# Performance work log

Hardware: AMD Instinct MI355X
Metric: run time of the kernel (lower is better)

The kernel has to match this reference:

```python
import jax, jax.numpy as jnp
import numpy as np

DEPTH, E, F, H, U, I, B = 12, 256, 128, 8, 1000, 1000, 64
HD = E // H  # head dim = 32
N = 2 * F + 1  # seq len = 257


def _ln(x, g, b, eps=1e-5):
    m = jnp.mean(x, axis=-1, keepdims=True)
    v = jnp.var(x, axis=-1, keepdims=True)
    return (x - m) / jnp.sqrt(v + eps) * g + b


def setup_inputs() -> dict:
    key = jax.random.key(0)
    ks = jax.random.split(key, 16)
    s = 0.02  # weight scale for numeric sanity
    inp = {
        "user": jax.random.randint(ks[0], (B, 1), 0, U, dtype=jnp.int64) if jax.config.jax_enable_x64 else jax.random.randint(ks[0], (B, 1), 0, U).astype(jnp.int32),
        "item": jax.random.randint(ks[1], (B, 1), 0, I).astype(jnp.int32),
        "user_table": jax.random.normal(ks[2], (E, U, F), jnp.float32) * s,
        "item_table": jax.random.normal(ks[3], (E, I, F), jnp.float32) * s,
        "cls_token": jax.random.normal(ks[4], (1, 1, E), jnp.float32),
        "positions": jax.random.normal(ks[5], (N, E), jnp.float32) * s,
        "ln1_g": jnp.ones((DEPTH, E), jnp.float32),
        "ln1_b": jnp.zeros((DEPTH, E), jnp.float32),
        "Wq": jax.random.normal(ks[6], (DEPTH, E, E), jnp.float32) * s,
        "bq": jnp.zeros((DEPTH, E), jnp.float32),
        "Wk": jax.random.normal(ks[7], (DEPTH, E, E), jnp.float32) * s,
        "bk": jnp.zeros((DEPTH, E), jnp.float32),
        "Wv": jax.random.normal(ks[8], (DEPTH, E, E), jnp.float32) * s,
        "bv": jnp.zeros((DEPTH, E), jnp.float32),
        "Wo": jax.random.normal(ks[9], (DEPTH, E, E), jnp.float32) * s,
        "bo": jnp.zeros((DEPTH, E), jnp.float32),
        "ln2_g": jnp.ones((DEPTH, E), jnp.float32),
        "ln2_b": jnp.zeros((DEPTH, E), jnp.float32),
        "W1": jax.random.normal(ks[10], (DEPTH, E, 4 * E), jnp.float32) * s,
        "b1": jnp.zeros((DEPTH, 4 * E), jnp.float32),
        "W2": jax.random.normal(ks[11], (DEPTH, 4 * E, E), jnp.float32) * s,
        "b2": jnp.zeros((DEPTH, E), jnp.float32),
        "head_g": jnp.ones((E,), jnp.float32),
        "head_b": jnp.zeros((E,), jnp.float32),
        "head_W": jax.random.normal(ks[12], (E, 1), jnp.float32) * s,
        "head_bias": jnp.zeros((1,), jnp.float32),
    }
    return inp


def _forward(user, item, user_table, item_table, cls_token, positions,
             ln1_g, ln1_b, Wq, bq, Wk, bk, Wv, bv, Wo, bo,
             ln2_g, ln2_b, W1, b1, W2, b2, head_g, head_b, head_W, head_bias):
    uid = user[:, 0]
    iid = item[:, 0]
    b = uid.shape[0]
    # emb_size parallel embedding lookups, cat over table axis, then transpose:
    # x_user[b, f, e] = user_table[e, uid[b], f]  -> (b, F, E)
    xu = jnp.transpose(user_table[:, uid, :], (1, 2, 0))
    xi = jnp.transpose(item_table[:, iid, :], (1, 2, 0))
    cls = jnp.broadcast_to(cls_token, (b, 1, E))
    x = jnp.concatenate([cls, xu, xi], axis=1) + positions  # (b, N, E)

    def block(x, p):
        g1, be1, wq, bq_, wk, bk_, wv, bv_, wo, bo_, g2, be2, w1, bb1, w2, bb2 = p
        h = _ln(x, g1, be1)

        def heads(w, bias):
            y = h @ w + bias  # (b, N, E)
            return y.reshape(b, N, H, HD).transpose(0, 2, 1, 3)  # (b, H, N, HD)

        q, k, v = heads(wq, bq_), heads(wk, bk_), heads(wv, bv_)
        energy = jnp.einsum('bhqd,bhkd->bhqk', q, k)  # NOTE: unscaled pre-softmax
        att = jax.nn.softmax(energy, axis=-1) / jnp.sqrt(jnp.float32(E))  # post-softmax scaling quirk
        o = jnp.einsum('bhqk,bhkd->bhqd', att, v)
        o = o.transpose(0, 2, 1, 3).reshape(b, N, E)
        x = x + (o @ wo + bo_)
        h2 = _ln(x, g2, be2)
        ff = jax.nn.gelu(h2 @ w1 + bb1, approximate=False) @ w2 + bb2
        return x + ff, None

    x, _ = jax.lax.scan(block, x, (ln1_g, ln1_b, Wq, bq, Wk, bk, Wv, bv, Wo, bo,
                                   ln2_g, ln2_b, W1, b1, W2, b2))
    pooled = jnp.mean(x, axis=1)  # (b, E)
    return _ln(pooled, head_g, head_b) @ head_W + head_bias  # (b, 1)


def reference(user, item, user_table, item_table, cls_token, positions,
              ln1_g, ln1_b, Wq, bq, Wk, bk, Wv, bv, Wo, bo,
              ln2_g, ln2_b, W1, b1, W2, b2, head_g, head_b, head_W, head_bias):
    return _forward(user, item, user_table, item_table, cls_token, positions,
                    ln1_g, ln1_b, Wq, bq, Wk, bk, Wv, bv, Wo, bo,
                    ln2_g, ln2_b, W1, b1, W2, b2, head_g, head_b, head_W, head_bias)
```

## Files before the change

kernel.cpp:

```cpp
#include <hip/hip_runtime.h>
#include <hip/hip_fp16.h>
#include <math.h>

constexpr int DEPTH = 12;
constexpr int E     = 256;
constexpr int H     = 8;
constexpr int HD    = 32;
constexpr int N     = 257;
constexpr int B     = 64;
constexpr int BN    = B * N;
constexpr int BNP   = 16512;
constexpr int FFD   = 1024;
constexpr int UCNT  = 1000;
constexpr int Fdim  = 128;

enum { EPI_RESID = 1, EPI_GELU = 2, EPI_QKV = 3 };

typedef _Float16 f16x8 __attribute__((ext_vector_type(8)));
typedef _Float16 f16x4 __attribute__((ext_vector_type(4)));
typedef float    f32x4 __attribute__((ext_vector_type(4)));

__device__ __forceinline__ float gelu_exact(float z) {
  return 0.5f * z * (1.0f + erff(z * 0.70710678118654752440f));
}

#define GLOAD_LDS16(g, l) __builtin_amdgcn_global_load_lds( \
    (const __attribute__((address_space(1))) void*)(g),     \
    (__attribute__((address_space(3))) void*)(l), 16, 0, 0)

__global__ __launch_bounds__(256) void embed_kernel(
    const int* __restrict__ user, const int* __restrict__ item,
    const float* __restrict__ utab, const float* __restrict__ itab,
    const float* __restrict__ pos, float* __restrict__ x)
{
  __shared__ float tile[32][33];
  const int tx = threadIdx.x, ty = threadIdx.y;
  const int b  = blockIdx.z;
  const int e0 = blockIdx.x * 32;
  const int ft = blockIdx.y;
  const bool isU = (ft < 4);
  const int f0 = (ft & 3) * 32;
  const int id = isU ? user[b] : item[b];
  const float* tab = isU ? utab : itab;
  const int nbase = isU ? 1 : 1 + Fdim;
#pragma unroll
  for (int r = 0; r < 4; ++r) {
    const int e = ty + r * 8;
    tile[e][tx] = tab[((size_t)(e0 + e) * UCNT + id) * Fdim + f0 + tx];
  }
  __syncthreads();
#pragma unroll
  for (int r = 0; r < 4; ++r) {
    const int f = ty + r * 8;
    const int n = nbase + f0 + f;
    x[((size_t)b * N + n) * E + e0 + tx] = tile[tx][f] + pos[(size_t)n * E + e0 + tx];
  }
}

__global__ __launch_bounds__(256) void cls_pad_kernel(
    const float* __restrict__ cls, const float* __restrict__ pos,
    float* __restrict__ x, __half* __restrict__ h)
{
  const int t = blockIdx.x * 256 + threadIdx.x;
  if (blockIdx.y == 0) {
    const int b = t >> 8, e = t & 255;
    x[((size_t)b * N) * E + e] = cls[e] + pos[e];
  } else {
    h[(size_t)BN * E + t] = __float2half(0.0f);
  }
}

__global__ __launch_bounds__(256) void convT_kernel(
    const float* __restrict__ in, __half* __restrict__ out,
    int K, int NC, int NCtot, int ncoff)
{
  __shared__ float tile[32][33];
  const int tx = threadIdx.x, ty = threadIdx.y;
  const int n0 = blockIdx.x * 32, k0 = blockIdx.y * 32;
  const float* ip = in + (size_t)blockIdx.z * K * NC;
  __half* op = out + (size_t)blockIdx.z * NCtot * K;
#pragma unroll
  for (int r = 0; r < 4; ++r) {
    const int kk = ty + r * 8;
    tile[kk][tx] = ip[(size_t)(k0 + kk) * NC + n0 + tx];
  }
  __syncthreads();
#pragma unroll
  for (int r = 0; r < 4; ++r) {
    const int nn = ty + r * 8;
    op[(size_t)(ncoff + n0 + nn) * K + k0 + tx] = __float2half(tile[tx][nn]);
  }
}

__global__ __launch_bounds__(256) void ln_kernel(
    const float* __restrict__ x, __half* __restrict__ y,
    const float* __restrict__ g, const float* __restrict__ b)
{
  const int wave = threadIdx.x >> 6, lane = threadIdx.x & 63;
  const int row  = blockIdx.x * 4 + wave;
  const float4 v = *(const float4*)(x + (size_t)row * E + lane * 4);
  float s = v.x + v.y + v.z + v.w;
  float q = v.x * v.x + v.y * v.y + v.z * v.z + v.w * v.w;
#pragma unroll
  for (int o = 32; o > 0; o >>= 1) { s += __shfl_xor(s, o); q += __shfl_xor(q, o); }
  const float mean = s * (1.0f / 256.0f);
  const float var  = q * (1.0f / 256.0f) - mean * mean;
  const float rstd = rsqrtf(var + 1e-5f);
  const float4 gg = *(const float4*)(g + lane * 4);
  const float4 bb = *(const float4*)(b + lane * 4);
  __half2 h0 = __floats2half2_rn((v.x - mean) * rstd * gg.x + bb.x,
                                 (v.y - mean) * rstd * gg.y + bb.y);
  __half2 h1 = __floats2half2_rn((v.z - mean) * rstd * gg.z + bb.z,
                                 (v.w - mean) * rstd * gg.w + bb.w);
  __half2* yp = (__half2*)(y + (size_t)row * E + lane * 4);
  yp[0] = h0; yp[1] = h1;
}

template<int BMC, int BNT, int K, int NCOUT, int EPI>
__global__ __launch_bounds__(256) void gemm_f16(
    const __half* __restrict__ Act, const __half* __restrict__ Wt,
    const float* __restrict__ b0, const float* __restrict__ b1,
    const float* __restrict__ b2, void* __restrict__ outp)
{
  static_assert(BMC == 128, "col tile fixed at 128");
  constexpr int NT  = BNT / 32;
  constexpr int BSEG = BNT / 16;
  constexpr int BPW  = BSEG / 4;

  __shared__ __half Ws[128 * 32];
  __shared__ __half Bs[BNT * 32];

  const int t = threadIdx.x;
  const int wave = t >> 6, lane = t & 63;
  const int lm = lane & 15, lq = lane >> 4;
  const int col0 = blockIdx.x * BMC;
  const int tok0 = blockIdx.y * BNT;

  const int srow = lane >> 2, sp = lane & 3;
  const __half* wg[2]; __half* wl[2];
#pragma unroll
  for (int i = 0; i < 2; ++i) {
    const int seg = wave * 2 + i;
    const int row = seg * 16 + srow;
    const int slot = sp ^ ((row >> 1) & 3);
    wg[i] = Wt + (size_t)(col0 + row) * K + slot * 8;
    wl[i] = &Ws[seg * 512];
  }
  const __half* ag[BPW]; __half* al[BPW];
#pragma unroll
  for (int i = 0; i < BPW; ++i) {
    const int seg = wave * BPW + i;
    const int row = seg * 16 + srow;
    const int slot = sp ^ ((row >> 1) & 3);
    ag[i] = Act + (size_t)(tok0 + row) * K + slot * 8;
    al[i] = &Bs[seg * 512];
  }

  const int wm = (wave >> 1) * 64;
  const int wn = (wave & 1) * (BNT / 2);

  f32x4 acc[4][NT];
#pragma unroll
  for (int i = 0; i < 4; ++i)
#pragma unroll
    for (int j = 0; j < NT; ++j) acc[i][j] = (f32x4){0.f, 0.f, 0.f, 0.f};

  for (int k0 = 0; k0 < K; k0 += 32) {
#pragma unroll
    for (int i = 0; i < 2; ++i)   GLOAD_LDS16(wg[i] + k0, wl[i]);
#pragma unroll
    for (int i = 0; i < BPW; ++i) GLOAD_LDS16(ag[i] + k0, al[i]);
    __syncthreads();

    f16x8 af[4], bf[NT];
#pragma unroll
    for (int mt = 0; mt < 4; ++mt) {
      const int row = wm + mt * 16 + lm;
      af[mt] = *(const f16x8*)&Ws[row * 32 + (lq ^ ((row >> 1) & 3)) * 8];
    }
#pragma unroll
    for (int nt = 0; nt < NT; ++nt) {
      const int row = wn + nt * 16 + lm;
      bf[nt] = *(const f16x8*)&Bs[row * 32 + (lq ^ ((row >> 1) & 3)) * 8];
    }
#pragma unroll
    for (int mt = 0; mt < 4; ++mt)
#pragma unroll
      for (int nt = 0; nt < NT; ++nt)
        acc[mt][nt] = __builtin_amdgcn_mfma_f32_16x16x32_f16(af[mt], bf[nt], acc[mt][nt], 0, 0, 0);
    __syncthreads();
  }

  float br[4][4];
#pragma unroll
  for (int mt = 0; mt < 4; ++mt) {
    const int cg = col0 + wm + mt * 16 + lq * 4;
    const float* bp;
    if constexpr (EPI == EPI_QKV) {
      const int tsel = cg >> 8;
      bp = (tsel == 0) ? b0 : (tsel == 1 ? b1 : b2);
      bp += (cg & 255);
    } else {
      bp = b0 + cg;
    }
    const float4 bv = *(const float4*)bp;
    br[mt][0] = bv.x; br[mt][1] = bv.y; br[mt][2] = bv.z; br[mt][3] = bv.w;
  }

#pragma unroll
  for (int nt = 0; nt < NT; ++nt) {
    const int token = tok0 + wn + nt * 16 + lm;
    if constexpr (EPI == EPI_RESID) {
      float* xrow = (float*)outp + (size_t)token * 256;
#pragma unroll
      for (int mt = 0; mt < 4; ++mt) {
        const int cg = col0 + wm + mt * 16 + lq * 4;
        float4 xv = *(float4*)(xrow + cg);
        xv.x += acc[mt][nt][0] + br[mt][0];
        xv.y += acc[mt][nt][1] + br[mt][1];
        xv.z += acc[mt][nt][2] + br[mt][2];
        xv.w += acc[mt][nt][3] + br[mt][3];
        *(float4*)(xrow + cg) = xv;
      }
    } else if constexpr (EPI == EPI_GELU) {
      if (token < BN) {
        __half* orow = (__half*)outp + (size_t)token * NCOUT;
#pragma unroll
        for (int mt = 0; mt < 4; ++mt) {
          const int cg = col0 + wm + mt * 16 + lq * 4;
          f16x4 hv;
#pragma unroll
          for (int r = 0; r < 4; ++r)
            hv[r] = (_Float16)gelu_exact(acc[mt][nt][r] + br[mt][r]);
          *(f16x4*)(orow + cg) = hv;
        }
      }
    } else {
      if (token < BN) {
        const unsigned tu = (unsigned)token;
        const unsigned bb = tu / 257u;
        const unsigned nn = tu - bb * 257u;
#pragma unroll
        for (int mt = 0; mt < 4; ++mt) {
          const int cg = col0 + wm + mt * 16 + lq * 4;
          const int tsel = cg >> 8, rc = cg & 255;
          __half* dst = (__half*)outp + (size_t)tsel * (BN * 256)
                      + (((size_t)bb * H + (rc >> 5)) * N + nn) * HD + (rc & 31);
          f16x4 hv;
#pragma unroll
          for (int r = 0; r < 4; ++r)
            hv[r] = (_Float16)(acc[mt][nt][r] + br[mt][r]);
          *(f16x4*)dst = hv;
        }
      }
    }
  }
}

__global__ __launch_bounds__(256) void attn_mfma(
    const __half* __restrict__ q, const __half* __restrict__ k,
    const __half* __restrict__ v, __half* __restrict__ o)
{
  __shared__ __align__(16) __half Ks[272][40];
  __shared__ __align__(16) __half Vt[32][280];

  const int bh = blockIdx.x;
  const int chunk = blockIdx.y;
  const int bb = bh >> 3, hh = bh & 7;
  const int t = threadIdx.x;
  const int wave = t >> 6, lane = t & 63;
  const int lm = lane & 15, lq = lane >> 4;

  const __half* kg = k + (size_t)bh * N * HD;
  const __half* vg = v + (size_t)bh * N * HD;

  const f16x8 zero8 = {0, 0, 0, 0, 0, 0, 0, 0};
  for (int i = t; i < 272 * 4; i += 256) {
    const int n = i >> 2, c8 = (i & 3) * 8;
    f16x8 kv = zero8, vv = zero8;
    if (n < N) {
      kv = *(const f16x8*)(kg + (size_t)n * HD + c8);
      vv = *(const f16x8*)(vg + (size_t)n * HD + c8);
    }
    *(f16x8*)&Ks[n][c8] = kv;
#pragma unroll
    for (int j = 0; j < 8; ++j) Vt[c8 + j][n] = vv[j];
  }
  __syncthreads();

  const int ntiles = chunk ? 8 : 9;
  const int tbase  = chunk ? 9 : 0;
  for (int ti = wave; ti < ntiles; ti += 4) {
    const int q0 = (tbase + ti) * 16;
    const int qg = q0 + lm;
    const int qrow = (qg < N) ? qg : (N - 1);
    const f16x8 bq = *(const f16x8*)(q + ((size_t)bh * N + qrow) * HD + lq * 8);
    f32x4 Ot0 = {0.f, 0.f, 0.f, 0.f}, Ot1 = {0.f, 0.f, 0.f, 0.f};
    float mm = -3.0e38f, ll = 0.0f;

    for (int kt = 0; kt < 17; ++kt) {
      const int k0 = kt * 16;
      const f16x8 ak = *(const f16x8*)&Ks[k0 + lm][lq * 8];
      f32x4 s = __builtin_amdgcn_mfma_f32_16x16x32_f16(ak, bq, (f32x4){0.f, 0.f, 0.f, 0.f}, 0, 0, 0);
      if (k0 == 256) {
        if (lq != 0) s[0] = -3.0e38f;
        s[1] = -3.0e38f; s[2] = -3.0e38f; s[3] = -3.0e38f;
      }
      float tm = fmaxf(fmaxf(s[0], s[1]), fmaxf(s[2], s[3]));
      tm = fmaxf(tm, __shfl_xor(tm, 16));
      tm = fmaxf(tm, __shfl_xor(tm, 32));
      const float mn    = fmaxf(mm, tm);
      const float alpha = __expf(mm - mn);
      const float p0 = __expf(s[0] - mn);
      const float p1 = __expf(s[1] - mn);
      const float p2 = __expf(s[2] - mn);
      const float p3 = __expf(s[3] - mn);
      float ts = p0 + p1 + p2 + p3;
      ts += __shfl_xor(ts, 16);
      ts += __shfl_xor(ts, 32);
      ll = ll * alpha + ts;
      Ot0 *= alpha;
      Ot1 *= alpha;
      const f16x4 pb = {(_Float16)p0, (_Float16)p1, (_Float16)p2, (_Float16)p3};
      const f16x4 av0 = *(const f16x4*)&Vt[lm][k0 + lq * 4];
      const f16x4 av1 = *(const f16x4*)&Vt[16 + lm][k0 + lq * 4];
      Ot0 = __builtin_amdgcn_mfma_f32_16x16x16f16(av0, pb, Ot0, 0, 0, 0);
      Ot1 = __builtin_amdgcn_mfma_f32_16x16x16f16(av1, pb, Ot1, 0, 0, 0);
      mm = mn;
    }

    const float inv = 1.0f / (16.0f * ll);
    if (qg < N) {
      __half* op = o + ((size_t)bb * N + qg) * E + hh * HD + lq * 4;
      __half2* p0 = (__half2*)op;
      p0[0] = __floats2half2_rn(Ot0[0] * inv, Ot0[1] * inv);
      p0[1] = __floats2half2_rn(Ot0[2] * inv, Ot0[3] * inv);
      __half2* p1 = (__half2*)(op + 16);
      p1[0] = __floats2half2_rn(Ot1[0] * inv, Ot1[1] * inv);
      p1[1] = __floats2half2_rn(Ot1[2] * inv, Ot1[3] * inv);
    }
  }
}

__global__ __launch_bounds__(256) void head_kernel(
    const float* __restrict__ x, const float* __restrict__ g,
    const float* __restrict__ bb, const float* __restrict__ hw,
    const float* __restrict__ hbias, float* __restrict__ out)
{
  const int b = blockIdx.x;
  const int e = threadIdx.x;
  const float* xp = x + (size_t)b * N * E + e;
  float s = 0.0f;
  for (int n = 0; n < N; ++n) s += xp[(size_t)n * E];
  const float p = s / 257.0f;

  float ls = p, lq = p * p;
#pragma unroll
  for (int o = 32; o > 0; o >>= 1) { ls += __shfl_xor(ls, o); lq += __shfl_xor(lq, o); }
  __shared__ float sm[4], sv[4], sd[4];
  const int wv = e >> 6, ln = e & 63;
  if (ln == 0) { sm[wv] = ls; sv[wv] = lq; }
  __syncthreads();
  const float mean = (sm[0] + sm[1] + sm[2] + sm[3]) * (1.0f / 256.0f);
  const float var  = (sv[0] + sv[1] + sv[2] + sv[3]) * (1.0f / 256.0f) - mean * mean;
  const float y = (p - mean) * rsqrtf(var + 1e-5f) * g[e] + bb[e];
  float d = y * hw[e];
#pragma unroll
  for (int o = 32; o > 0; o >>= 1) d += __shfl_xor(d, o);
  if (ln == 0) sd[wv] = d;
  __syncthreads();
  if (e == 0) out[b] = sd[0] + sd[1] + sd[2] + sd[3] + hbias[0];
}

extern "C" void kernel_launch(void* const* d_in, const int* in_sizes, int n_in,
                              void* d_out, int out_size, void* d_ws, size_t ws_size,
                              hipStream_t stream)
{
  const int*   user = (const int*)d_in[0];
  const int*   item = (const int*)d_in[1];
  const float* utab = (const float*)d_in[2];
  const float* itab = (const float*)d_in[3];
  const float* cls  = (const float*)d_in[4];
  const float* pos  = (const float*)d_in[5];
  const float* ln1g = (const float*)d_in[6];
  const float* ln1b = (const float*)d_in[7];
  const float* Wq   = (const float*)d_in[8];
  const float* bq   = (const float*)d_in[9];
  const float* Wk   = (const float*)d_in[10];
  const float* bk   = (const float*)d_in[11];
  const float* Wv   = (const float*)d_in[12];
  const float* bv   = (const float*)d_in[13];
  const float* Wo   = (const float*)d_in[14];
  const float* bo   = (const float*)d_in[15];
  const float* ln2g = (const float*)d_in[16];
  const float* ln2b = (const float*)d_in[17];
  const float* W1   = (const float*)d_in[18];
  const float* b1   = (const float*)d_in[19];
  const float* W2   = (const float*)d_in[20];
  const float* b2   = (const float*)d_in[21];
  const float* hg   = (const float*)d_in[22];
  const float* hb   = (const float*)d_in[23];
  const float* hW   = (const float*)d_in[24];
  const float* hbias= (const float*)d_in[25];
  float* out = (float*)d_out;

  float*  x  = (float*)d_ws;
  __half* h  = (__half*)(x + (size_t)BN * E);
  __half* fq = h + (size_t)BNP * E;
  __half* Wqkvt = fq + (size_t)BN * FFD;
  __half* Wot   = Wqkvt + (size_t)DEPTH * 768 * 256;
  __half* W1t   = Wot   + (size_t)DEPTH * 256 * 256;
  __half* W2t   = W1t   + (size_t)DEPTH * 1024 * 256;
  __half* qb = fq;
  __half* kb = fq + (size_t)BN * 256;
  __half* vb = fq + (size_t)2 * BN * 256;

  convT_kernel<<<dim3(8, 8, DEPTH),  dim3(32, 8), 0, stream>>>(Wq, Wqkvt, 256, 256, 768, 0);
  convT_kernel<<<dim3(8, 8, DEPTH),  dim3(32, 8), 0, stream>>>(Wk, Wqkvt, 256, 256, 768, 256);
  convT_kernel<<<dim3(8, 8, DEPTH),  dim3(32, 8), 0, stream>>>(Wv, Wqkvt, 256, 256, 768, 512);
  convT_kernel<<<dim3(8, 8, DEPTH),  dim3(32, 8), 0, stream>>>(Wo, Wot, 256, 256, 256, 0);
  convT_kernel<<<dim3(32, 8, DEPTH), dim3(32, 8), 0, stream>>>(W1, W1t, 256, 1024, 1024, 0);
  convT_kernel<<<dim3(8, 32, DEPTH), dim3(32, 8), 0, stream>>>(W2, W2t, 1024, 256, 256, 0);

  cls_pad_kernel<<<dim3(64, 2), 256, 0, stream>>>(cls, pos, x, h);
  embed_kernel<<<dim3(8, 8, B), dim3(32, 8), 0, stream>>>(user, item, utab, itab, pos, x);

  for (int L = 0; L < DEPTH; ++L) {
    ln_kernel<<<BN / 4, 256, 0, stream>>>(x, h, ln1g + L * E, ln1b + L * E);
    gemm_f16<128, 128, 256, 768, EPI_QKV><<<dim3(6, 129), 256, 0, stream>>>(
        h, Wqkvt + (size_t)L * 768 * 256, bq + L * E, bk + L * E, bv + L * E, fq);
    attn_mfma<<<dim3(512, 2), 256, 0, stream>>>(qb, kb, vb, h);
    gemm_f16<128, 64, 256, 256, EPI_RESID><<<dim3(2, 257), 256, 0, stream>>>(
        h, Wot + (size_t)L * 256 * 256, bo + L * E, bo + L * E, bo + L * E, x);
    ln_kernel<<<BN / 4, 256, 0, stream>>>(x, h, ln2g + L * E, ln2b + L * E);
    gemm_f16<128, 128, 256, 1024, EPI_GELU><<<dim3(8, 129), 256, 0, stream>>>(
        h, W1t + (size_t)L * 1024 * 256, b1 + (size_t)L * FFD, b1 + (size_t)L * FFD, b1 + (size_t)L * FFD, fq);
    gemm_f16<128, 64, 1024, 256, EPI_RESID><<<dim3(2, 257), 256, 0, stream>>>(
        fq, W2t + (size_t)L * 256 * 1024, b2 + L * E, b2 + L * E, b2 + L * E, x);
  }

  head_kernel<<<B, 256, 0, stream>>>(x, hg, hb, hW, hbias, out);
}
```

Measured before the change: 1.753 ms.

## Fuse LayerNorm into residual GEMM epilogues and double-buffer GEMM LDS staging

The Wo and W2 residual GEMMs now use a full 256-column tile, so each block owns complete rows. Their epilogue adds the residual, reduces mean and variance across waves through shared memory, and writes the LayerNorm'd fp16 activations for the next stage. This removes the separate ln_kernel launches and the extra pass over x. The GEMM main loop also double-buffers its LDS tiles with explicit vmcnt waits, so the next k-step's loads overlap the MFMAs. The trade-off is fewer blocks for the residual GEMMs, which lowers parallelism, and the last layer's fused LN output is computed but never used.

```diff
diff --git a/kernel.cpp b/kernel.cpp
--- a/kernel.cpp
+++ b/kernel.cpp
@@ -14,7 +14,7 @@
 constexpr int UCNT  = 1000;
 constexpr int Fdim  = 128;
 
-enum { EPI_RESID = 1, EPI_GELU = 2, EPI_QKV = 3 };
+enum { EPI_RESID = 1, EPI_GELU = 2, EPI_QKV = 3, EPI_RESID_LN = 4 };
 
 typedef _Float16 f16x8 __attribute__((ext_vector_type(8)));
 typedef _Float16 f16x4 __attribute__((ext_vector_type(4)));
@@ -27,6 +27,14 @@
 #define GLOAD_LDS16(g, l) __builtin_amdgcn_global_load_lds( \
     (const __attribute__((address_space(1))) void*)(g),     \
     (__attribute__((address_space(3))) void*)(l), 16, 0, 0)
+
+template<int NV>
+__device__ __forceinline__ void wait_vmcnt() {
+  static_assert(NV == 0 || NV == 4 || NV == 5, "unsupported vmcnt literal");
+  if constexpr (NV == 0)      asm volatile("s_waitcnt vmcnt(0)" ::: "memory");
+  else if constexpr (NV == 4) asm volatile("s_waitcnt vmcnt(4)" ::: "memory");
+  else                        asm volatile("s_waitcnt vmcnt(5)" ::: "memory");
+}
 
 __global__ __launch_bounds__(256) void embed_kernel(
     const int* __restrict__ user, const int* __restrict__ item,
@@ -120,15 +128,24 @@
 __global__ __launch_bounds__(256) void gemm_f16(
     const __half* __restrict__ Act, const __half* __restrict__ Wt,
     const float* __restrict__ b0, const float* __restrict__ b1,
-    const float* __restrict__ b2, void* __restrict__ outp)
-{
-  static_assert(BMC == 128, "col tile fixed at 128");
-  constexpr int NT  = BNT / 32;
-  constexpr int BSEG = BNT / 16;
-  constexpr int BPW  = BSEG / 4;
-
-  __shared__ __half Ws[128 * 32];
-  __shared__ __half Bs[BNT * 32];
+    const float* __restrict__ b2,
+    const float* __restrict__ lng, const float* __restrict__ lnb,
+    __half* __restrict__ hout, void* __restrict__ outp)
+{
+  constexpr int WAVES_M = BMC / 64;
+  constexpr int WAVES_N = 4 / WAVES_M;
+  constexpr int MT = 4;
+  constexpr int NT = BNT / (16 * WAVES_N);
+  constexpr int ASW = (BMC / 16) / 4;
+  constexpr int BSW = (BNT / 16) / 4;
+  constexpr int NDMA = ASW + BSW;
+  constexpr int AHALF = BMC * 32;
+  constexpr int BHALF = BNT * 32;
+  constexpr int BUF   = AHALF + BHALF;
+  constexpr int NSTEP = K / 32;
+  static_assert(NT == 4 && MT == 4, "acc shape fixed");
+
+  __shared__ __align__(16) __half smem[2 * BUF];
 
   const int t = threadIdx.x;
   const int wave = t >> 6, lane = t & 63;
@@ -137,46 +154,58 @@
   const int tok0 = blockIdx.y * BNT;
 
   const int srow = lane >> 2, sp = lane & 3;
-  const __half* wg[2]; __half* wl[2];
-#pragma unroll
-  for (int i = 0; i < 2; ++i) {
-    const int seg = wave * 2 + i;
+  const __half* ag[ASW]; int aoff[ASW];
+#pragma unroll
+  for (int i = 0; i < ASW; ++i) {
+    const int seg = wave * ASW + i;
     const int row = seg * 16 + srow;
     const int slot = sp ^ ((row >> 1) & 3);
-    wg[i] = Wt + (size_t)(col0 + row) * K + slot * 8;
-    wl[i] = &Ws[seg * 512];
-  }
-  const __half* ag[BPW]; __half* al[BPW];
-#pragma unroll
-  for (int i = 0; i < BPW; ++i) {
-    const int seg = wave * BPW + i;
+    ag[i] = Wt + (size_t)(col0 + row) * K + slot * 8;
+    aoff[i] = seg * 512;
+  }
+  const __half* bg[BSW]; int boff[BSW];
+#pragma unroll
+  for (int i = 0; i < BSW; ++i) {
+    const int seg = wave * BSW + i;
     const int row = seg * 16 + srow;
     const int slot = sp ^ ((row >> 1) & 3);
-    ag[i] = Act + (size_t)(tok0 + row) * K + slot * 8;
-    al[i] = &Bs[seg * 512];
-  }
-
-  const int wm = (wave >> 1) * 64;
-  const int wn = (wave & 1) * (BNT / 2);
-
-  f32x4 acc[4][NT];
-#pragma unroll
-  for (int i = 0; i < 4; ++i)
+    bg[i] = Act + (size_t)(tok0 + row) * K + slot * 8;
+    boff[i] = seg * 512;
+  }
+
+  auto STAGE = [&](int step, int buf) {
+    const int koff = step * 32;
+    __half* base = smem + buf * BUF;
+#pragma unroll
+    for (int i = 0; i < ASW; ++i) GLOAD_LDS16(ag[i] + koff, base + aoff[i]);
+#pragma unroll
+    for (int i = 0; i < BSW; ++i) GLOAD_LDS16(bg[i] + koff, base + AHALF + boff[i]);
+  };
+
+  const int wm = (wave / WAVES_N) * 64;
+  const int wn = (wave % WAVES_N) * (16 * NT);
+
+  f32x4 acc[MT][NT];
+#pragma unroll
+  for (int i = 0; i < MT; ++i)
 #pragma unroll
     for (int j = 0; j < NT; ++j) acc[i][j] = (f32x4){0.f, 0.f, 0.f, 0.f};
 
-  for (int k0 = 0; k0 < K; k0 += 32) {
-#pragma unroll
-    for (int i = 0; i < 2; ++i)   GLOAD_LDS16(wg[i] + k0, wl[i]);
-#pragma unroll
-    for (int i = 0; i < BPW; ++i) GLOAD_LDS16(ag[i] + k0, al[i]);
-    __syncthreads();
-
-    f16x8 af[4], bf[NT];
-#pragma unroll
-    for (int mt = 0; mt < 4; ++mt) {
+  STAGE(0, 0);
+  for (int s = 0; s < NSTEP; ++s) {
+    const int cur = s & 1;
+    if (s + 1 < NSTEP) { STAGE(s + 1, cur ^ 1); wait_vmcnt<NDMA>(); }
+    else               { wait_vmcnt<0>(); }
+    __builtin_amdgcn_s_barrier();
+    asm volatile("" ::: "memory");
+
+    const __half* As = smem + cur * BUF;
+    const __half* Bs = As + AHALF;
+    f16x8 af[MT], bf[NT];
+#pragma unroll
+    for (int mt = 0; mt < MT; ++mt) {
       const int row = wm + mt * 16 + lm;
-      af[mt] = *(const f16x8*)&Ws[row * 32 + (lq ^ ((row >> 1) & 3)) * 8];
+      af[mt] = *(const f16x8*)&As[row * 32 + (lq ^ ((row >> 1) & 3)) * 8];
     }
 #pragma unroll
     for (int nt = 0; nt < NT; ++nt) {
@@ -184,16 +213,20 @@
       bf[nt] = *(const f16x8*)&Bs[row * 32 + (lq ^ ((row >> 1) & 3)) * 8];
     }
 #pragma unroll
-    for (int mt = 0; mt < 4; ++mt)
+    for (int mt = 0; mt < MT; ++mt)
 #pragma unroll
       for (int nt = 0; nt < NT; ++nt)
         acc[mt][nt] = __builtin_amdgcn_mfma_f32_16x16x32_f16(af[mt], bf[nt], acc[mt][nt], 0, 0, 0);
-    __syncthreads();
-  }
-
-  float br[4][4];
-#pragma unroll
-  for (int mt = 0; mt < 4; ++mt) {
+
+    if (s + 1 < NSTEP || EPI == EPI_RESID_LN) {
+      __builtin_amdgcn_s_barrier();
+      asm volatile("" ::: "memory");
+    }
+  }
+
+  float br[MT][4];
+#pragma unroll
+  for (int mt = 0; mt < MT; ++mt) {
     const int cg = col0 + wm + mt * 16 + lq * 4;
     const float* bp;
     if constexpr (EPI == EPI_QKV) {
@@ -207,50 +240,109 @@
     br[mt][0] = bv.x; br[mt][1] = bv.y; br[mt][2] = bv.z; br[mt][3] = bv.w;
   }
 
-#pragma unroll
-  for (int nt = 0; nt < NT; ++nt) {
-    const int token = tok0 + wn + nt * 16 + lm;
-    if constexpr (EPI == EPI_RESID) {
+  if constexpr (EPI == EPI_RESID_LN) {
+    float* sred = (float*)smem;
+    float* qred = sred + 256;
+#pragma unroll
+    for (int nt = 0; nt < NT; ++nt) {
+      const int tl = wn + nt * 16 + lm;
+      const int token = tok0 + tl;
       float* xrow = (float*)outp + (size_t)token * 256;
-#pragma unroll
-      for (int mt = 0; mt < 4; ++mt) {
-        const int cg = col0 + wm + mt * 16 + lq * 4;
-        float4 xv = *(float4*)(xrow + cg);
-        xv.x += acc[mt][nt][0] + br[mt][0];
-        xv.y += acc[mt][nt][1] + br[mt][1];
-        xv.z += acc[mt][nt][2] + br[mt][2];
-        xv.w += acc[mt][nt][3] + br[mt][3];
-        *(float4*)(xrow + cg) = xv;
+      float s = 0.f, q = 0.f;
+#pragma unroll
+      for (int mt = 0; mt < MT; ++mt) {
+        const int cg = wm + mt * 16 + lq * 4;
+        const float4 xv = *(const float4*)(xrow + cg);
+        float v0 = acc[mt][nt][0] + br[mt][0] + xv.x;
+        float v1 = acc[mt][nt][1] + br[mt][1] + xv.y;
+        float v2 = acc[mt][nt][2] + br[mt][2] + xv.z;
+        float v3 = acc[mt][nt][3] + br[mt][3] + xv.w;
+        acc[mt][nt][0] = v0; acc[mt][nt][1] = v1;
+        acc[mt][nt][2] = v2; acc[mt][nt][3] = v3;
+        s += v0 + v1 + v2 + v3;
+        q += v0 * v0 + v1 * v1 + v2 * v2 + v3 * v3;
+        float4 nv; nv.x = v0; nv.y = v1; nv.z = v2; nv.w = v3;
+        *(float4*)(xrow + cg) = nv;
       }
-    } else if constexpr (EPI == EPI_GELU) {
-      if (token < BN) {
-        __half* orow = (__half*)outp + (size_t)token * NCOUT;
-#pragma unroll
-        for (int mt = 0; mt < 4; ++mt) {
+      s += __shfl_xor(s, 16); s += __shfl_xor(s, 32);
+      q += __shfl_xor(q, 16); q += __shfl_xor(q, 32);
+      if (lq == 0) { sred[wave * 64 + tl] = s; qred[wave * 64 + tl] = q; }
+    }
+    __syncthreads();
+    float4 g4[MT], e4[MT];
+#pragma unroll
+    for (int mt = 0; mt < MT; ++mt) {
+      const int cg = wm + mt * 16 + lq * 4;
+      g4[mt] = *(const float4*)(lng + cg);
+      e4[mt] = *(const float4*)(lnb + cg);
+    }
+#pragma unroll
+    for (int nt = 0; nt < NT; ++nt) {
+      const int tl = wn + nt * 16 + lm;
+      const int token = tok0 + tl;
+      const float ts = sred[tl] + sred[64 + tl] + sred[128 + tl] + sred[192 + tl];
+      const float tq = qred[tl] + qred[64 + tl] + qred[128 + tl] + qred[192 + tl];
+      const float mean = ts * (1.0f / 256.0f);
+      const float var  = tq * (1.0f / 256.0f) - mean * mean;
+      const float rstd = rsqrtf(var + 1e-5f);
+      __half* hrow = hout + (size_t)token * 256;
+#pragma unroll
+      for (int mt = 0; mt < MT; ++mt) {
+        const int cg = wm + mt * 16 + lq * 4;
+        f16x4 hv;
+        hv[0] = (_Float16)((acc[mt][nt][0] - mean) * rstd * g4[mt].x + e4[mt].x);
+        hv[1] = (_Float16)((acc[mt][nt][1] - mean) * rstd * g4[mt].y + e4[mt].y);
+        hv[2] = (_Float16)((acc[mt][nt][2] - mean) * rstd * g4[mt].z + e4[mt].z);
+        hv[3] = (_Float16)((acc[mt][nt][3] - mean) * rstd * g4[mt].w + e4[mt].w);
+        *(f16x4*)(hrow + cg) = hv;
+      }
+    }
+  } else {
+#pragma unroll
+    for (int nt = 0; nt < NT; ++nt) {
+      const int token = tok0 + wn + nt * 16 + lm;
+      if constexpr (EPI == EPI_RESID) {
+        float* xrow = (float*)outp + (size_t)token * 256;
+#pragma unroll
+        for (int mt = 0; mt < MT; ++mt) {
           const int cg = col0 + wm + mt * 16 + lq * 4;
-          f16x4 hv;
-#pragma unroll
-          for (int r = 0; r < 4; ++r)
-            hv[r] = (_Float16)gelu_exact(acc[mt][nt][r] + br[mt][r]);
-          *(f16x4*)(orow + cg) = hv;
+          float4 xv = *(float4*)(xrow + cg);
+          xv.x += acc[mt][nt][0] + br[mt][0];
+          xv.y += acc[mt][nt][1] + br[mt][1];
+          xv.z += acc[mt][nt][2] + br[mt][2];
+          xv.w += acc[mt][nt][3] + br[mt][3];
+          *(float4*)(xrow + cg) = xv;
         }
-      }
-    } else {
-      if (token < BN) {
-        const unsigned tu = (unsigned)token;
-        const unsigned bb = tu / 257u;
-        const unsigned nn = tu - bb * 257u;
-#pragma unroll
-        for (int mt = 0; mt < 4; ++mt) {
-          const int cg = col0 + wm + mt * 16 + lq * 4;
-          const int tsel = cg >> 8, rc = cg & 255;
-          __half* dst = (__half*)outp + (size_t)tsel * (BN * 256)
-                      + (((size_t)bb * H + (rc >> 5)) * N + nn) * HD + (rc & 31);
-          f16x4 hv;
-#pragma unroll
-          for (int r = 0; r < 4; ++r)
-            hv[r] = (_Float16)(acc[mt][nt][r] + br[mt][r]);
-          *(f16x4*)dst = hv;
+      } else if constexpr (EPI == EPI_GELU) {
+        if (token < BN) {
+          __half* orow = (__half*)outp + (size_t)token * NCOUT;
+#pragma unroll
+          for (int mt = 0; mt < MT; ++mt) {
+            const int cg = col0 + wm + mt * 16 + lq * 4;
+            f16x4 hv;
+#pragma unroll
+            for (int r = 0; r < 4; ++r)
+              hv[r] = (_Float16)gelu_exact(acc[mt][nt][r] + br[mt][r]);
+            *(f16x4*)(orow + cg) = hv;
+          }
+        }
+      } else {
+        if (token < BN) {
+          const unsigned tu = (unsigned)token;
+          const unsigned bb = tu / 257u;
+          const unsigned nn = tu - bb * 257u;
+#pragma unroll
+          for (int mt = 0; mt < MT; ++mt) {
+            const int cg = col0 + wm + mt * 16 + lq * 4;
+            const int tsel = cg >> 8, rc = cg & 255;
+            __half* dst = (__half*)outp + (size_t)tsel * (BN * 256)
+                        + (((size_t)bb * H + (rc >> 5)) * N + nn) * HD + (rc & 31);
+            f16x4 hv;
+#pragma unroll
+            for (int r = 0; r < 4; ++r)
+              hv[r] = (_Float16)(acc[mt][nt][r] + br[mt][r]);
+            *(f16x4*)dst = hv;
+          }
         }
       }
     }
@@ -424,19 +516,25 @@
 
   cls_pad_kernel<<<dim3(64, 2), 256, 0, stream>>>(cls, pos, x, h);
   embed_kernel<<<dim3(8, 8, B), dim3(32, 8), 0, stream>>>(user, item, utab, itab, pos, x);
+  ln_kernel<<<BN / 4, 256, 0, stream>>>(x, h, ln1g, ln1b);
 
   for (int L = 0; L < DEPTH; ++L) {
-    ln_kernel<<<BN / 4, 256, 0, stream>>>(x, h, ln1g + L * E, ln1b + L * E);
+    const float* g1n = ln1g + (size_t)((L + 1) % DEPTH) * E;
+    const float* b1n = ln1b + (size_t)((L + 1) % DEPTH) * E;
+
     gemm_f16<128, 128, 256, 768, EPI_QKV><<<dim3(6, 129), 256, 0, stream>>>(
-        h, Wqkvt + (size_t)L * 768 * 256, bq + L * E, bk + L * E, bv + L * E, fq);
+        h, Wqkvt + (size_t)L * 768 * 256, bq + L * E, bk + L * E, bv + L * E,
+        nullptr, nullptr, nullptr, fq);
     attn_mfma<<<dim3(512, 2), 256, 0, stream>>>(qb, kb, vb, h);
-    gemm_f16<128, 64, 256, 256, EPI_RESID><<<dim3(2, 257), 256, 0, stream>>>(
-        h, Wot + (size_t)L * 256 * 256, bo + L * E, bo + L * E, bo + L * E, x);
-    ln_kernel<<<BN / 4, 256, 0, stream>>>(x, h, ln2g + L * E, ln2b + L * E);
+    gemm_f16<256, 64, 256, 256, EPI_RESID_LN><<<dim3(1, 257), 256, 0, stream>>>(
+        h, Wot + (size_t)L * 256 * 256, bo + L * E, nullptr, nullptr,
+        ln2g + L * E, ln2b + L * E, h, x);
     gemm_f16<128, 128, 256, 1024, EPI_GELU><<<dim3(8, 129), 256, 0, stream>>>(
-        h, W1t + (size_t)L * 1024 * 256, b1 + (size_t)L * FFD, b1 + (size_t)L * FFD, b1 + (size_t)L * FFD, fq);
-    gemm_f16<128, 64, 1024, 256, EPI_RESID><<<dim3(2, 257), 256, 0, stream>>>(
-        fq, W2t + (size_t)L * 256 * 1024, b2 + L * E, b2 + L * E, b2 + L * E, x);
+        h, W1t + (size_t)L * 1024 * 256, b1 + (size_t)L * FFD, nullptr, nullptr,
+        nullptr, nullptr, nullptr, fq);
+    gemm_f16<256, 64, 1024, 256, EPI_RESID_LN><<<dim3(1, 257), 256, 0, stream>>>(
+        fq, W2t + (size_t)L * 256 * 1024, b2 + L * E, nullptr, nullptr,
+        g1n, b1n, h, x);
   }
 
   head_kernel<<<B, 256, 0, stream>>>(x, hg, hb, hW, hbias, out);
```

Measured after the change: 1.777 ms. Within noise of the previous version (+1.3%).

## Double-buffer GEMM LDS tiles and remap blocks across XCDs

Applied to the files above, without the earlier changes.

The GEMM kernel now double-buffers its shared-memory tiles. It issues the async global-to-LDS loads for the next k-step before computing the current one, and uses vmcnt waits with raw barriers in place of two __syncthreads per step. The 2D grid is flattened to 1D and block ids are remapped so each group of 8 consecutive ids (one per XCD) covers contiguous tiles, which should improve L2 locality on the multi-XCD chip. LDS use doubles, which may reduce occupancy.

```diff
diff --git a/kernel.cpp b/kernel.cpp
--- a/kernel.cpp
+++ b/kernel.cpp
@@ -27,6 +27,11 @@
 #define GLOAD_LDS16(g, l) __builtin_amdgcn_global_load_lds( \
     (const __attribute__((address_space(1))) void*)(g),     \
     (__attribute__((address_space(3))) void*)(l), 16, 0, 0)
+
+template<int NV>
+__device__ __forceinline__ void wait_vmcnt() {
+  asm volatile("s_waitcnt vmcnt(%0)" :: "i"(NV) : "memory");
+}
 
 __global__ __launch_bounds__(256) void embed_kernel(
     const int* __restrict__ user, const int* __restrict__ item,
@@ -116,67 +121,90 @@
   yp[0] = h0; yp[1] = h1;
 }
 
-template<int BMC, int BNT, int K, int NCOUT, int EPI>
+template<int BMC, int BNT, int K, int NCOUT, int EPI, int NX>
 __global__ __launch_bounds__(256) void gemm_f16(
     const __half* __restrict__ Act, const __half* __restrict__ Wt,
     const float* __restrict__ b0, const float* __restrict__ b1,
     const float* __restrict__ b2, void* __restrict__ outp)
 {
-  static_assert(BMC == 128, "col tile fixed at 128");
-  constexpr int NT  = BNT / 32;
-  constexpr int BSEG = BNT / 16;
-  constexpr int BPW  = BSEG / 4;
-
-  __shared__ __half Ws[128 * 32];
-  __shared__ __half Bs[BNT * 32];
+  constexpr int MT = 4;
+  constexpr int NT = BNT / 32;
+  constexpr int ASW = (BMC / 16) / 4;
+  constexpr int BSW = (BNT / 16) / 4;
+  constexpr int NDMA = ASW + BSW;
+  constexpr int AHALF = BMC * 32;
+  constexpr int BHALF = BNT * 32;
+  constexpr int BUF   = AHALF + BHALF;
+  constexpr int NSTEP = K / 32;
+
+  __shared__ __align__(16) __half smem[2 * BUF];
 
   const int t = threadIdx.x;
   const int wave = t >> 6, lane = t & 63;
   const int lm = lane & 15, lq = lane >> 4;
-  const int col0 = blockIdx.x * BMC;
-  const int tok0 = blockIdx.y * BNT;
+
+  const int wid = blockIdx.x;
+  const int total = gridDim.x;
+  const int q8 = total >> 3, r8 = total & 7;
+  const int c = wid & 7, j = wid >> 3;
+  const int lin = c * q8 + (c < r8 ? c : r8) + j;
+  const int bx = lin % NX, by = lin / NX;
+  const int col0 = bx * BMC;
+  const int tok0 = by * BNT;
 
   const int srow = lane >> 2, sp = lane & 3;
-  const __half* wg[2]; __half* wl[2];
-#pragma unroll
-  for (int i = 0; i < 2; ++i) {
-    const int seg = wave * 2 + i;
+  const __half* ag[ASW]; int aoff[ASW];
+#pragma unroll
+  for (int i = 0; i < ASW; ++i) {
+    const int seg = wave * ASW + i;
     const int row = seg * 16 + srow;
     const int slot = sp ^ ((row >> 1) & 3);
-    wg[i] = Wt + (size_t)(col0 + row) * K + slot * 8;
-    wl[i] = &Ws[seg * 512];
-  }
-  const __half* ag[BPW]; __half* al[BPW];
-#pragma unroll
-  for (int i = 0; i < BPW; ++i) {
-    const int seg = wave * BPW + i;
+    ag[i] = Wt + (size_t)(col0 + row) * K + slot * 8;
+    aoff[i] = seg * 512;
+  }
+  const __half* bg[BSW]; int boff[BSW];
+#pragma unroll
+  for (int i = 0; i < BSW; ++i) {
+    const int seg = wave * BSW + i;
     const int row = seg * 16 + srow;
     const int slot = sp ^ ((row >> 1) & 3);
-    ag[i] = Act + (size_t)(tok0 + row) * K + slot * 8;
-    al[i] = &Bs[seg * 512];
-  }
+    bg[i] = Act + (size_t)(tok0 + row) * K + slot * 8;
+    boff[i] = seg * 512;
+  }
+
+  auto STAGE = [&](int step, int buf) {
+    const int koff = step * 32;
+    __half* base = smem + buf * BUF;
+#pragma unroll
+    for (int i = 0; i < ASW; ++i) GLOAD_LDS16(ag[i] + koff, base + aoff[i]);
+#pragma unroll
+    for (int i = 0; i < BSW; ++i) GLOAD_LDS16(bg[i] + koff, base + AHALF + boff[i]);
+  };
 
   const int wm = (wave >> 1) * 64;
   const int wn = (wave & 1) * (BNT / 2);
 
-  f32x4 acc[4][NT];
-#pragma unroll
-  for (int i = 0; i < 4; ++i)
-#pragma unroll
-    for (int j = 0; j < NT; ++j) acc[i][j] = (f32x4){0.f, 0.f, 0.f, 0.f};
-
-  for (int k0 = 0; k0 < K; k0 += 32) {
-#pragma unroll
-    for (int i = 0; i < 2; ++i)   GLOAD_LDS16(wg[i] + k0, wl[i]);
-#pragma unroll
-    for (int i = 0; i < BPW; ++i) GLOAD_LDS16(ag[i] + k0, al[i]);
-    __syncthreads();
-
-    f16x8 af[4], bf[NT];
-#pragma unroll
-    for (int mt = 0; mt < 4; ++mt) {
+  f32x4 acc[MT][NT];
+#pragma unroll
+  for (int i = 0; i < MT; ++i)
+#pragma unroll
+    for (int j2 = 0; j2 < NT; ++j2) acc[i][j2] = (f32x4){0.f, 0.f, 0.f, 0.f};
+
+  STAGE(0, 0);
+  for (int s = 0; s < NSTEP; ++s) {
+    const int cur = s & 1;
+    if (s + 1 < NSTEP) { STAGE(s + 1, cur ^ 1); wait_vmcnt<NDMA>(); }
+    else               { wait_vmcnt<0>(); }
+    __builtin_amdgcn_s_barrier();
+    asm volatile("" ::: "memory");
+
+    const __half* As = smem + cur * BUF;
+    const __half* Bs = As + AHALF;
+    f16x8 af[MT], bf[NT];
+#pragma unroll
+    for (int mt = 0; mt < MT; ++mt) {
       const int row = wm + mt * 16 + lm;
-      af[mt] = *(const f16x8*)&Ws[row * 32 + (lq ^ ((row >> 1) & 3)) * 8];
+      af[mt] = *(const f16x8*)&As[row * 32 + (lq ^ ((row >> 1) & 3)) * 8];
     }
 #pragma unroll
     for (int nt = 0; nt < NT; ++nt) {
@@ -184,16 +212,20 @@
       bf[nt] = *(const f16x8*)&Bs[row * 32 + (lq ^ ((row >> 1) & 3)) * 8];
     }
 #pragma unroll
-    for (int mt = 0; mt < 4; ++mt)
+    for (int mt = 0; mt < MT; ++mt)
 #pragma unroll
       for (int nt = 0; nt < NT; ++nt)
         acc[mt][nt] = __builtin_amdgcn_mfma_f32_16x16x32_f16(af[mt], bf[nt], acc[mt][nt], 0, 0, 0);
-    __syncthreads();
-  }
-
-  float br[4][4];
-#pragma unroll
-  for (int mt = 0; mt < 4; ++mt) {
+
+    if (s + 1 < NSTEP) {
+      __builtin_amdgcn_s_barrier();
+      asm volatile("" ::: "memory");
+    }
+  }
+
+  float br[MT][4];
+#pragma unroll
+  for (int mt = 0; mt < MT; ++mt) {
     const int cg = col0 + wm + mt * 16 + lq * 4;
     const float* bp;
     if constexpr (EPI == EPI_QKV) {
@@ -213,7 +245,7 @@
     if constexpr (EPI == EPI_RESID) {
       float* xrow = (float*)outp + (size_t)token * 256;
 #pragma unroll
-      for (int mt = 0; mt < 4; ++mt) {
+      for (int mt = 0; mt < MT; ++mt) {
         const int cg = col0 + wm + mt * 16 + lq * 4;
         float4 xv = *(float4*)(xrow + cg);
         xv.x += acc[mt][nt][0] + br[mt][0];
@@ -226,7 +258,7 @@
       if (token < BN) {
         __half* orow = (__half*)outp + (size_t)token * NCOUT;
 #pragma unroll
-        for (int mt = 0; mt < 4; ++mt) {
+        for (int mt = 0; mt < MT; ++mt) {
           const int cg = col0 + wm + mt * 16 + lq * 4;
           f16x4 hv;
 #pragma unroll
@@ -241,7 +273,7 @@
         const unsigned bb = tu / 257u;
         const unsigned nn = tu - bb * 257u;
 #pragma unroll
-        for (int mt = 0; mt < 4; ++mt) {
+        for (int mt = 0; mt < MT; ++mt) {
           const int cg = col0 + wm + mt * 16 + lq * 4;
           const int tsel = cg >> 8, rc = cg & 255;
           __half* dst = (__half*)outp + (size_t)tsel * (BN * 256)
@@ -427,16 +459,16 @@
 
   for (int L = 0; L < DEPTH; ++L) {
     ln_kernel<<<BN / 4, 256, 0, stream>>>(x, h, ln1g + L * E, ln1b + L * E);
-    gemm_f16<128, 128, 256, 768, EPI_QKV><<<dim3(6, 129), 256, 0, stream>>>(
+    gemm_f16<128, 128, 256, 768, EPI_QKV, 6><<<774, 256, 0, stream>>>(
         h, Wqkvt + (size_t)L * 768 * 256, bq + L * E, bk + L * E, bv + L * E, fq);
     attn_mfma<<<dim3(512, 2), 256, 0, stream>>>(qb, kb, vb, h);
-    gemm_f16<128, 64, 256, 256, EPI_RESID><<<dim3(2, 257), 256, 0, stream>>>(
-        h, Wot + (size_t)L * 256 * 256, bo + L * E, bo + L * E, bo + L * E, x);
+    gemm_f16<128, 64, 256, 256, EPI_RESID, 2><<<514, 256, 0, stream>>>(
+        h, Wot + (size_t)L * 256 * 256, bo + L * E, nullptr, nullptr, x);
     ln_kernel<<<BN / 4, 256, 0, stream>>>(x, h, ln2g + L * E, ln2b + L * E);
-    gemm_f16<128, 128, 256, 1024, EPI_GELU><<<dim3(8, 129), 256, 0, stream>>>(
-        h, W1t + (size_t)L * 1024 * 256, b1 + (size_t)L * FFD, b1 + (size_t)L * FFD, b1 + (size_t)L * FFD, fq);
-    gemm_f16<128, 64, 1024, 256, EPI_RESID><<<dim3(2, 257), 256, 0, stream>>>(
-        fq, W2t + (size_t)L * 256 * 1024, b2 + L * E, b2 + L * E, b2 + L * E, x);
+    gemm_f16<128, 128, 256, 1024, EPI_GELU, 8><<<1032, 256, 0, stream>>>(
+        h, W1t + (size_t)L * 1024 * 256, b1 + (size_t)L * FFD, nullptr, nullptr, fq);
+    gemm_f16<128, 64, 1024, 256, EPI_RESID, 2><<<514, 256, 0, stream>>>(
+        fq, W2t + (size_t)L * 256 * 1024, b2 + L * E, nullptr, nullptr, x);
   }
 
   head_kernel<<<B, 256, 0, stream>>>(x, hg, hb, hW, hbias, out);
```

Measured after the change: 1.648 ms. 6.0% less time.
